# Optimization experiments

Measured on AMD Instinct MI355X. Metric: run time of the kernel, lower is better.

The kernel has to match this reference:

```python
import jax, jax.numpy as jnp
import numpy as np

H = 1024
W = 1024
SAMPLES_PER_SEG = 32
SIGMA_AA = 1.0
EDGE_CHUNK = 32  # matches torch chunk_size


def sample_bezier_path(control_points):
    # control_points: [N, 2], N = 3*S + 1 cubic segments
    N = control_points.shape[0]
    S = (N - 1) // 3
    idx = 3 * jnp.arange(S)
    p0 = control_points[idx][:, None, :]      # [S,1,2]
    p1 = control_points[idx + 1][:, None, :]
    p2 = control_points[idx + 2][:, None, :]
    p3 = control_points[idx + 3][:, None, :]
    t = jnp.linspace(0.0, 1.0, SAMPLES_PER_SEG, dtype=control_points.dtype)[None, :, None]  # [1,T,1]
    mt = 1.0 - t
    pts = (mt * mt * mt) * p0 + 3.0 * (mt * mt) * t * p1 + 3.0 * mt * (t * t) * p2 + (t * t * t) * p3
    return pts.reshape(S * SAMPLES_PER_SEG, 2)  # [M,2]


def compute_winding(path_points, sigma):
    # path_points: [M,2]; closed polygon edges (j -> (j+1)%M)
    M = path_points.shape[0]
    nxt = jnp.roll(path_points, -1, axis=0)
    x0, y0 = path_points[:, 0], path_points[:, 1]
    x1, y1 = nxt[:, 0], nxt[:, 1]
    dy = y1 - y0
    dx = x1 - x0
    # edges with |dy| < 1e-6 are skipped in the original (continue) -> zero contribution
    coeff = jnp.sign(dy) * (jnp.abs(dy) >= 1e-6).astype(path_points.dtype)
    grid_y = jnp.arange(H, dtype=path_points.dtype)  # rows
    grid_x = jnp.arange(W, dtype=path_points.dtype)  # cols

    n_chunks = M // EDGE_CHUNK
    def chunk_it(a):
        return a.reshape(n_chunks, EDGE_CHUNK)

    def body(acc, c):
        cx0, cy0, cdy, cdx, cc = c  # each [CH]
        t_cross = (grid_y[None, :] - cy0[:, None]) / (cdy[:, None] + 1e-8)          # [CH,H]
        x_cross = cx0[:, None] + t_cross * cdx[:, None]                              # [CH,H]
        valid_t = jax.nn.sigmoid(t_cross * 20.0) * jax.nn.sigmoid((1.0 - t_cross) * 20.0)  # [CH,H]
        crosses = jax.nn.sigmoid((x_cross[:, :, None] - grid_x[None, None, :]) / sigma)    # [CH,H,W]
        contrib = jnp.sum(crosses * (valid_t * cc[:, None])[:, :, None], axis=0)           # [H,W]
        return acc + contrib, None

    init = jnp.zeros((H, W), dtype=path_points.dtype)
    winding, _ = jax.lax.scan(body, init, (chunk_it(x0), chunk_it(y0), chunk_it(dy), chunk_it(dx), chunk_it(coeff)))
    return winding


def setup_inputs() -> dict:
    key = jax.random.key(0)
    k1, k2 = jax.random.split(key)
    control_points = jax.random.uniform(k1, (49, 2), dtype=jnp.float32) * jnp.float32(W)
    color = jax.random.uniform(k2, (3,), dtype=jnp.float32)
    return {"control_points": control_points, "color": color}


def reference(control_points, color):
    pts = sample_bezier_path(control_points)          # [M,2]
    winding = compute_winding(pts, SIGMA_AA)          # [H,W]
    alpha = jax.nn.sigmoid(winding * 4.0)             # [H,W]
    rgb = jnp.broadcast_to(color[None, None, :], (H, W, 3))
    rgba = jnp.concatenate([rgb, alpha[..., None]], axis=-1)  # [H,W,4]
    return rgba
```

## Files before the change

kernel.cpp:

```cpp
#include <hip/hip_runtime.h>

#define HH 1024
#define WW 1024
#define NPTS 512
#define TPB 1024
#define W_EPS 1e-6f
#define CAP 32

__device__ __forceinline__ float sigmoidf(float z) {
    float e = __expf(-z);
    return __builtin_amdgcn_rcpf(1.0f + e);
}

__device__ __forceinline__ float2 bez(const float* cpL, int i) {
    i &= (NPTS - 1);
    int seg = i >> 5;
    int j = i & 31;
    float t = (float)j * (1.0f / 31.0f);
    float mt = 1.0f - t;
    int b = 6 * seg;
    float a0 = mt * mt * mt;
    float a1 = 3.0f * mt * mt * t;
    float a2 = 3.0f * mt * t * t;
    float a3 = t * t * t;
    return make_float2(
        a0 * cpL[b+0] + a1 * cpL[b+2] + a2 * cpL[b+4] + a3 * cpL[b+6],
        a0 * cpL[b+1] + a1 * cpL[b+3] + a2 * cpL[b+5] + a3 * cpL[b+7]);
}

__global__ __launch_bounds__(TPB) void render_kernel(
    const float* __restrict__ cp,
    const float* __restrict__ color,
    float* __restrict__ out)
{
    __shared__ float  cpL[98];
    __shared__ float  colL[3];
    __shared__ float2 actXW[NPTS];
    __shared__ int    actTMM[NPTS];
    __shared__ float2 bucket[16][CAP];
    __shared__ int    cnt[16];
    __shared__ int    n_act;

    const int tid = threadIdx.x;
    const int y = blockIdx.x;
    const float yf = (float)y;

    if (tid < 98) cpL[tid] = cp[tid];
    if (tid < 3)  colL[tid] = color[tid];
    if (tid == 0) n_act = 0;
    if (tid < 16) cnt[tid] = 0;
    __syncthreads();

    if (tid < NPTS) {
        float2 p = bez(cpL, tid);
        float2 q = bez(cpL, tid + 1);
        float dy = q.y - p.y;
        float dx = q.x - p.x;
        float c = (dy > 0.0f) ? 1.0f : ((dy < 0.0f) ? -1.0f : 0.0f);
        if (fabsf(dy) < 1e-6f) c = 0.0f;
        float t = (yf - p.y) * __builtin_amdgcn_rcpf(dy + 1e-8f);
        float vt = sigmoidf(t * 20.0f) * sigmoidf((1.0f - t) * 20.0f);
        float w = vt * c;
        if (fabsf(w) > W_EPS) {
            float xc = fmaf(t, dx, p.x);
            int tmin = (int)ceilf((xc - 77.0f) * 0.015625f);
            tmin = max(0, min(16, tmin));
            int tmax = (int)floorf((xc + 14.0f) * 0.015625f);
            tmax = max(-1, min(15, tmax));
            int idx = atomicAdd(&n_act, 1);
            actXW[idx] = make_float2(xc, w);
            actTMM[idx] = tmin | ((tmax + 1) << 8);
            for (int tt = tmin; tt <= tmax; ++tt) {
                int pos = atomicAdd(&cnt[tt], 1);
                if (pos < CAP) bucket[tt][pos] = make_float2(xc, w);
            }
        }
    }
    __syncthreads();

    const int t = tid >> 6;
    const int lane = tid & 63;
    const int n = n_act;
    const float xf = (float)(t * 64 + lane);

    float sat = 0.0f;
    for (int i = lane; i < n; i += 64) {
        int tmin = actTMM[i] & 0xff;
        if (t < tmin) sat += actXW[i].y;
    }
    #pragma unroll
    for (int o = 32; o > 0; o >>= 1) sat += __shfl_xor(sat, o);

    float acc;
    const int m = cnt[t];
    if (m <= CAP) {
        acc = sat;
        for (int j = 0; j < m; ++j) {
            float2 d = bucket[t][j];
            acc = fmaf(d.y, sigmoidf(d.x - xf), acc);
        }
    } else {
        acc = 0.0f;
        for (int i = 0; i < n; ++i) {
            int tmm = actTMM[i];
            int tmin = tmm & 0xff;
            int tmax = (tmm >> 8) - 1;
            if (t < tmin) {
                acc += actXW[i].y;
            } else if (t <= tmax) {
                float2 d = actXW[i];
                acc = fmaf(d.y, sigmoidf(d.x - xf), acc);
            }
        }
    }

    float4* orow = ((float4*)out) + y * WW;
    orow[tid] = make_float4(colL[0], colL[1], colL[2], sigmoidf(4.0f * acc));
}

extern "C" void kernel_launch(void* const* d_in, const int* in_sizes, int n_in,
                              void* d_out, int out_size, void* d_ws, size_t ws_size,
                              hipStream_t stream) {
    const float* cp = (const float*)d_in[0];
    const float* color = (const float*)d_in[1];
    float* out = (float*)d_out;
    render_kernel<<<HH, TPB, 0, stream>>>(cp, color, out);
}
```

Baseline: 65.76 us.

## Split rendering into per-row edge prep kernel and quarter-row render kernel

Moves per-row edge crossing computation into a separate prep kernel that writes compacted active-edge lists to workspace. A second kernel then renders each row with four 256-thread blocks instead of one 1024-thread block. The per-tile bucketing and saturation reduction are dropped in favour of a single loop over all active edges with a tile-range test. The aim is more blocks and better occupancy, at the cost of an extra launch, a workspace round trip, and a per-thread loop over every active edge.

Result: slower. 73.04 us (+11.1%).

```diff
diff --git a/kernel.cpp b/kernel.cpp
--- a/kernel.cpp
+++ b/kernel.cpp
@@ -3,9 +3,8 @@
 #define HH 1024
 #define WW 1024
 #define NPTS 512
-#define TPB 1024
 #define W_EPS 1e-6f
-#define CAP 32
+#define ROWSTRIDE (NPTS + 1)
 
 __device__ __forceinline__ float sigmoidf(float z) {
     float e = __expf(-z);
@@ -28,30 +27,23 @@
         a0 * cpL[b+1] + a1 * cpL[b+3] + a2 * cpL[b+5] + a3 * cpL[b+7]);
 }
 
-__global__ __launch_bounds__(TPB) void render_kernel(
+__global__ __launch_bounds__(512) void prep_kernel(
     const float* __restrict__ cp,
-    const float* __restrict__ color,
-    float* __restrict__ out)
+    float4* __restrict__ ws)
 {
     __shared__ float  cpL[98];
-    __shared__ float  colL[3];
-    __shared__ float2 actXW[NPTS];
-    __shared__ int    actTMM[NPTS];
-    __shared__ float2 bucket[16][CAP];
-    __shared__ int    cnt[16];
+    __shared__ float4 act[NPTS];
     __shared__ int    n_act;
 
     const int tid = threadIdx.x;
     const int y = blockIdx.x;
     const float yf = (float)y;
 
+    if (tid == 0) n_act = 0;
     if (tid < 98) cpL[tid] = cp[tid];
-    if (tid < 3)  colL[tid] = color[tid];
-    if (tid == 0) n_act = 0;
-    if (tid < 16) cnt[tid] = 0;
     __syncthreads();
 
-    if (tid < NPTS) {
+    {
         float2 p = bez(cpL, tid);
         float2 q = bez(cpL, tid + 1);
         float dy = q.y - p.y;
@@ -68,54 +60,52 @@
             int tmax = (int)floorf((xc + 14.0f) * 0.015625f);
             tmax = max(-1, min(15, tmax));
             int idx = atomicAdd(&n_act, 1);
-            actXW[idx] = make_float2(xc, w);
-            actTMM[idx] = tmin | ((tmax + 1) << 8);
-            for (int tt = tmin; tt <= tmax; ++tt) {
-                int pos = atomicAdd(&cnt[tt], 1);
-                if (pos < CAP) bucket[tt][pos] = make_float2(xc, w);
-            }
+            act[idx] = make_float4(xc, w, (float)tmin, (float)tmax);
         }
     }
     __syncthreads();
 
-    const int t = tid >> 6;
+    float4* row = ws + y * ROWSTRIDE;
+    const int n = n_act;
+    if (tid == 0) *(int*)row = n;
+    if (tid < n) row[1 + tid] = act[tid];
+}
+
+__global__ __launch_bounds__(256) void render_kernel(
+    const float4* __restrict__ ws,
+    const float* __restrict__ color,
+    float* __restrict__ out)
+{
+    __shared__ float4 list[NPTS];
+
+    const int tid = threadIdx.x;
+    const int y = blockIdx.x >> 2;
+    const int quarter = blockIdx.x & 3;
+    const float4* rp = ws + y * ROWSTRIDE;
+
+    const int n = *(const int*)rp;
+    for (int i = tid; i < n; i += 256) list[i] = rp[1 + i];
+    __syncthreads();
+
+    const int t = quarter * 4 + (tid >> 6);
     const int lane = tid & 63;
-    const int n = n_act;
     const float xf = (float)(t * 64 + lane);
 
-    float sat = 0.0f;
-    for (int i = lane; i < n; i += 64) {
-        int tmin = actTMM[i] & 0xff;
-        if (t < tmin) sat += actXW[i].y;
-    }
-    #pragma unroll
-    for (int o = 32; o > 0; o >>= 1) sat += __shfl_xor(sat, o);
-
-    float acc;
-    const int m = cnt[t];
-    if (m <= CAP) {
-        acc = sat;
-        for (int j = 0; j < m; ++j) {
-            float2 d = bucket[t][j];
-            acc = fmaf(d.y, sigmoidf(d.x - xf), acc);
-        }
-    } else {
-        acc = 0.0f;
-        for (int i = 0; i < n; ++i) {
-            int tmm = actTMM[i];
-            int tmin = tmm & 0xff;
-            int tmax = (tmm >> 8) - 1;
-            if (t < tmin) {
-                acc += actXW[i].y;
-            } else if (t <= tmax) {
-                float2 d = actXW[i];
-                acc = fmaf(d.y, sigmoidf(d.x - xf), acc);
-            }
+    float acc = 0.0f;
+    for (int i = 0; i < n; ++i) {
+        float4 e = list[i];
+        int tmin = (int)e.z;
+        int tmax = (int)e.w;
+        if (t < tmin) {
+            acc += e.y;
+        } else if (t <= tmax) {
+            acc = fmaf(e.y, sigmoidf(e.x - xf), acc);
         }
     }
 
     float4* orow = ((float4*)out) + y * WW;
-    orow[tid] = make_float4(colL[0], colL[1], colL[2], sigmoidf(4.0f * acc));
+    orow[t * 64 + lane] = make_float4(color[0], color[1], color[2],
+                                      sigmoidf(4.0f * acc));
 }
 
 extern "C" void kernel_launch(void* const* d_in, const int* in_sizes, int n_in,
@@ -124,5 +114,8 @@
     const float* cp = (const float*)d_in[0];
     const float* color = (const float*)d_in[1];
     float* out = (float*)d_out;
-    render_kernel<<<HH, TPB, 0, stream>>>(cp, color, out);
+    float4* ws = (float4*)d_ws;
+
+    prep_kernel<<<HH, 512, 0, stream>>>(cp, ws);
+    render_kernel<<<HH * 4, 256, 0, stream>>>(ws, color, out);
 }
```

## Split each row into four 256-pixel blocks with single per-block crossing list

Applied to the files above, without the earlier changes.

Launches four 256-thread blocks per row instead of one 1024-thread block. Each block keeps only the edge crossings near its quarter-row, in one shared list, and sums the crossings to its right into a single saturated weight. This drops the 16 per-tile buckets and the per-thread saturation loop, which cuts shared atomics and serial work. In exchange, every block recomputes the 512 Bezier samples and edge crossings, so that setup work is repeated four times per row.

Result: no change. 66.63 us (+1.3%).

```diff
diff --git a/kernel.cpp b/kernel.cpp
--- a/kernel.cpp
+++ b/kernel.cpp
@@ -3,9 +3,9 @@
 #define HH 1024
 #define WW 1024
 #define NPTS 512
-#define TPB 1024
+#define TPB 256
 #define W_EPS 1e-6f
-#define CAP 32
+#define CAP 64
 
 __device__ __forceinline__ float sigmoidf(float z) {
     float e = __expf(-z);
@@ -13,7 +13,6 @@
 }
 
 __device__ __forceinline__ float2 bez(const float* cpL, int i) {
-    i &= (NPTS - 1);
     int seg = i >> 5;
     int j = i & 31;
     float t = (float)j * (1.0f / 31.0f);
@@ -35,27 +34,35 @@
 {
     __shared__ float  cpL[98];
     __shared__ float  colL[3];
-    __shared__ float2 actXW[NPTS];
-    __shared__ int    actTMM[NPTS];
-    __shared__ float2 bucket[16][CAP];
-    __shared__ int    cnt[16];
-    __shared__ int    n_act;
+    __shared__ float2 ptsL[NPTS];
+    __shared__ float2 list[CAP];
+    __shared__ int    n_list;
+    __shared__ float  satW;
 
     const int tid = threadIdx.x;
-    const int y = blockIdx.x;
+    const int y = blockIdx.x >> 2;
+    const int q = blockIdx.x & 3;
     const float yf = (float)y;
+    const float qlo = (float)(q * 256);
+    const float qhi = qlo + 255.0f;
 
     if (tid < 98) cpL[tid] = cp[tid];
     if (tid < 3)  colL[tid] = color[tid];
-    if (tid == 0) n_act = 0;
-    if (tid < 16) cnt[tid] = 0;
+    if (tid == 0) { n_list = 0; satW = 0.0f; }
     __syncthreads();
 
-    if (tid < NPTS) {
-        float2 p = bez(cpL, tid);
-        float2 q = bez(cpL, tid + 1);
-        float dy = q.y - p.y;
-        float dx = q.x - p.x;
+    ptsL[tid]       = bez(cpL, tid);
+    ptsL[tid + 256] = bez(cpL, tid + 256);
+    __syncthreads();
+
+    float mySat = 0.0f;
+    #pragma unroll
+    for (int k = 0; k < 2; ++k) {
+        int e = tid + k * 256;
+        float2 p = ptsL[e];
+        float2 qq = ptsL[(e + 1) & (NPTS - 1)];
+        float dy = qq.y - p.y;
+        float dx = qq.x - p.x;
         float c = (dy > 0.0f) ? 1.0f : ((dy < 0.0f) ? -1.0f : 0.0f);
         if (fabsf(dy) < 1e-6f) c = 0.0f;
         float t = (yf - p.y) * __builtin_amdgcn_rcpf(dy + 1e-8f);
@@ -63,59 +70,50 @@
         float w = vt * c;
         if (fabsf(w) > W_EPS) {
             float xc = fmaf(t, dx, p.x);
-            int tmin = (int)ceilf((xc - 77.0f) * 0.015625f);
-            tmin = max(0, min(16, tmin));
-            int tmax = (int)floorf((xc + 14.0f) * 0.015625f);
-            tmax = max(-1, min(15, tmax));
-            int idx = atomicAdd(&n_act, 1);
-            actXW[idx] = make_float2(xc, w);
-            actTMM[idx] = tmin | ((tmax + 1) << 8);
-            for (int tt = tmin; tt <= tmax; ++tt) {
-                int pos = atomicAdd(&cnt[tt], 1);
-                if (pos < CAP) bucket[tt][pos] = make_float2(xc, w);
+            if (xc >= qhi + 14.0f) {
+                mySat += w;
+            } else if (xc > qlo - 14.0f) {
+                int pos = atomicAdd(&n_list, 1);
+                if (pos < CAP) list[pos] = make_float2(xc, w);
             }
         }
     }
+    #pragma unroll
+    for (int o = 32; o > 0; o >>= 1) mySat += __shfl_xor(mySat, o);
+    if ((tid & 63) == 0) atomicAdd(&satW, mySat);
     __syncthreads();
 
-    const int t = tid >> 6;
-    const int lane = tid & 63;
-    const int n = n_act;
-    const float xf = (float)(t * 64 + lane);
-
-    float sat = 0.0f;
-    for (int i = lane; i < n; i += 64) {
-        int tmin = actTMM[i] & 0xff;
-        if (t < tmin) sat += actXW[i].y;
-    }
-    #pragma unroll
-    for (int o = 32; o > 0; o >>= 1) sat += __shfl_xor(sat, o);
-
+    const float xf = qlo + (float)tid;
+    const int n = n_list;
     float acc;
-    const int m = cnt[t];
-    if (m <= CAP) {
-        acc = sat;
-        for (int j = 0; j < m; ++j) {
-            float2 d = bucket[t][j];
+    if (n <= CAP) {
+        acc = satW;
+        for (int i = 0; i < n; ++i) {
+            float2 d = list[i];
             acc = fmaf(d.y, sigmoidf(d.x - xf), acc);
         }
     } else {
         acc = 0.0f;
-        for (int i = 0; i < n; ++i) {
-            int tmm = actTMM[i];
-            int tmin = tmm & 0xff;
-            int tmax = (tmm >> 8) - 1;
-            if (t < tmin) {
-                acc += actXW[i].y;
-            } else if (t <= tmax) {
-                float2 d = actXW[i];
-                acc = fmaf(d.y, sigmoidf(d.x - xf), acc);
+        for (int e = 0; e < NPTS; ++e) {
+            float2 p = ptsL[e];
+            float2 qq = ptsL[(e + 1) & (NPTS - 1)];
+            float dy = qq.y - p.y;
+            float dx = qq.x - p.x;
+            float c = (dy > 0.0f) ? 1.0f : ((dy < 0.0f) ? -1.0f : 0.0f);
+            if (fabsf(dy) < 1e-6f) c = 0.0f;
+            float t = (yf - p.y) * __builtin_amdgcn_rcpf(dy + 1e-8f);
+            float vt = sigmoidf(t * 20.0f) * sigmoidf((1.0f - t) * 20.0f);
+            float w = vt * c;
+            if (fabsf(w) > W_EPS) {
+                float xc = fmaf(t, dx, p.x);
+                acc = fmaf(w, sigmoidf(xc - xf), acc);
             }
         }
     }
 
     float4* orow = ((float4*)out) + y * WW;
-    orow[tid] = make_float4(colL[0], colL[1], colL[2], sigmoidf(4.0f * acc));
+    orow[q * 256 + tid] = make_float4(colL[0], colL[1], colL[2],
+                                      sigmoidf(4.0f * acc));
 }
 
 extern "C" void kernel_launch(void* const* d_in, const int* in_sizes, int n_in,
@@ -124,5 +122,5 @@
     const float* cp = (const float*)d_in[0];
     const float* color = (const float*)d_in[1];
     float* out = (float*)d_out;
-    render_kernel<<<HH, TPB, 0, stream>>>(cp, color, out);
+    render_kernel<<<HH * 4, TPB, 0, stream>>>(cp, color, out);
 }
```
